# Kernel tuning notes

Measured on AMD Instinct MI355X. Metric: run time of the kernel, lower is better.

## Reference

```python
import jax, jax.numpy as jnp
import numpy as np

K = 20
HID = 64
NUM_CLASSES = 50
BIG = 1e10  # effectively-infinite distance for self-loop exclusion


def knn_idx(x, k):
    # x: [N, d] -> idx: [N, k] indices of k nearest neighbors in feature space (excluding self)
    sq = jnp.sum(x * x, axis=1)
    dist = sq[:, None] + sq[None, :] - 2.0 * (x @ x.T)  # [N, N]
    n = x.shape[0]
    dist = dist.at[jnp.arange(n), jnp.arange(n)].set(BIG)
    _, idx = jax.lax.top_k(-dist, k)
    return idx


def edge_conv(x, k, W, b):
    # DynamicEdgeConv: message = relu(Linear(cat[x_i, x_j - x_i])), aggr = max over k neighbors
    idx = knn_idx(x, k)                      # [N, k]
    xj = x[idx]                              # [N, k, d] neighbor gather
    xi = jnp.broadcast_to(x[:, None, :], xj.shape)
    feat = jnp.concatenate([xi, xj - xi], axis=-1)   # [N, k, 2d]
    h = jax.nn.relu(jnp.einsum('nkf,fo->nko', feat, W) + b)
    return jnp.max(h, axis=1)                # [N, out]


def setup_inputs() -> dict:
    key = jax.random.key(0)
    ks = jax.random.split(key, 16)
    def lin(kw, fan_in, fan_out):
        s = 1.0 / np.sqrt(fan_in)
        return jax.random.uniform(kw, (fan_in, fan_out), jnp.float32, -s, s)
    inp = {
        'x':  jax.random.normal(ks[0], (8192, 3), jnp.float32),
        'W1': lin(ks[1], 2 * 3, HID),      'b1': jnp.zeros((HID,), jnp.float32),
        'W2': lin(ks[2], 2 * HID, HID),    'b2': jnp.zeros((HID,), jnp.float32),
        'W3': lin(ks[3], 2 * HID, HID),    'b3': jnp.zeros((HID,), jnp.float32),
        'Wl': lin(ks[4], 3 * HID, 1024),   'bl': jnp.zeros((1024,), jnp.float32),
        'Wm1': lin(ks[5], 1024, 256),      'bm1': jnp.zeros((256,), jnp.float32),
        'Wm2': lin(ks[6], 256, 128),       'bm2': jnp.zeros((128,), jnp.float32),
        'Wo': lin(ks[7], 128, NUM_CLASSES),'bo': jnp.zeros((NUM_CLASSES,), jnp.float32),
    }
    return inp


def reference(x, W1, b1, W2, b2, W3, b3, Wl, bl, Wm1, bm1, Wm2, bm2, Wo, bo):
    x1 = edge_conv(x, K, W1, b1)     # [N, 64], kNN on raw 3-D points
    x2 = edge_conv(x1, K, W2, b2)    # [N, 64], kNN recomputed in feature space
    x3 = edge_conv(x2, K, W3, b3)    # [N, 64]
    h = jnp.concatenate([x1, x2, x3], axis=1)            # [N, 192]
    h = jax.nn.relu(h @ Wl + bl)                         # lin1: MLP([192, 1024])
    h = jax.nn.relu(h @ Wm1 + bm1)                       # MLP([1024, 256]) (dropout: eval mode)
    h = jax.nn.relu(h @ Wm2 + bm2)                       # MLP([256, 128])
    out = h @ Wo + bo                                    # final Linear
    return jax.nn.log_softmax(out, axis=-1)
```

## Files before the change

### kernel.cpp

```cpp
#include <hip/hip_runtime.h>
#include <math.h>

#define NPTS 8192
#define KNN 20
#define NLISTS 32
#define JSPLIT 8

#define OFF_SQ   0
#define OFF_IDX  8192
#define OFF_A    172032
#define OFF_B    696320
#define OFF_CAT  1220608
#define OFF_H1   2793472
#define OFF_H2   11182080
#define OFF_H3   13279232
#define OFF_PART OFF_H1
#define OFF_PACK (OFF_H1 + 5242880)
#define PACK_ELEMS 262144
#define OFF_WT   OFF_A

typedef __attribute__((ext_vector_type(8))) short bf16x8;
typedef __attribute__((ext_vector_type(16))) float f32x16;

__device__ inline unsigned umed3(unsigned a, unsigned b, unsigned c) {
    unsigned d;
    asm("v_med3_u32 %0, %1, %2, %3" : "=v"(d) : "v"(a), "v"(b), "v"(c));
    return d;
}

__device__ inline unsigned short f2bf(float f) {
    unsigned u = __float_as_uint(f);
    u += 0x7FFFu + ((u >> 16) & 1u);
    return (unsigned short)(u >> 16);
}

template<int D>
__global__ __launch_bounds__(256)
void sqnorm_kernel(const float* __restrict__ X, int stride, float* __restrict__ sq) {
    int n = blockIdx.x * blockDim.x + threadIdx.x;
    if (n < NPTS) {
        float s = 0.f;
        #pragma unroll
        for (int f = 0; f < D; ++f) {
            float v = X[(size_t)n * stride + f];
            s = fmaf(v, v, s);
        }
        sq[n] = s;
    }
}

template<int D, int KP>
__global__ __launch_bounds__(256)
void prepack_kernel(const float* __restrict__ X, int stride,
                    unsigned short* __restrict__ Xhi, unsigned short* __restrict__ Xlo,
                    unsigned short* __restrict__ Yhi, unsigned short* __restrict__ Ylo) {
    int t2 = blockIdx.x * 256 + threadIdx.x;
    int t = t2 * 2;
    int n = t >> (KP == 64 ? 6 : 4);
    int k = t & (KP - 1);
    float xv[2];
    xv[0] = (k     < D) ? X[(size_t)n * stride + k]     : 0.f;
    xv[1] = (k + 1 < D) ? X[(size_t)n * stride + k + 1] : 0.f;
    ushort2 hx, lx, hy, ly;
    unsigned short* hxp = (unsigned short*)&hx;
    unsigned short* lxp = (unsigned short*)&lx;
    unsigned short* hyp = (unsigned short*)&hy;
    unsigned short* lyp = (unsigned short*)&ly;
    #pragma unroll
    for (int e = 0; e < 2; ++e) {
        float x = xv[e];
        unsigned short hi = f2bf(x);
        float hif = __uint_as_float((unsigned)hi << 16);
        unsigned short lo = f2bf(x - hif);
        float y = -2.f * x;
        unsigned short yhi = f2bf(y);
        float yhif = __uint_as_float((unsigned)yhi << 16);
        unsigned short ylo = f2bf(y - yhif);
        hxp[e] = hi; lxp[e] = lo; hyp[e] = yhi; lyp[e] = ylo;
    }
    *(ushort2*)&Xhi[t] = hx;
    *(ushort2*)&Xlo[t] = lx;
    *(ushort2*)&Yhi[t] = hy;
    *(ushort2*)&Ylo[t] = ly;
}

template<int K, int NBITS>
__global__ __launch_bounds__(256)
void prepack_w(const float* __restrict__ W,
               unsigned short* __restrict__ Thi, unsigned short* __restrict__ Tlo) {
    const int N = 1 << NBITS;
    int t = blockIdx.x * 256 + threadIdx.x;
    int k = t >> NBITS, n = t & (N - 1);
    float x = W[t];
    unsigned short hi = f2bf(x);
    float hif = __uint_as_float((unsigned)hi << 16);
    unsigned short lo = f2bf(x - hif);
    Thi[(size_t)n * K + k] = hi;
    Tlo[(size_t)n * K + k] = lo;
}

template<int KP>
__global__ __launch_bounds__(256, 4)
void knnA_mfma(const unsigned short* __restrict__ Yhi, const unsigned short* __restrict__ Ylo,
               const unsigned short* __restrict__ Xhi, const unsigned short* __restrict__ Xlo,
               const float* __restrict__ sq, unsigned int* __restrict__ part) {
    constexpr int NS = KP / 16;
    constexpr int NT = NPTS / JSPLIT / 4 / 32;
    const int wave = threadIdx.x >> 6, lane = threadIdx.x & 63;
    const int col = lane & 31;
    const int h   = lane >> 5;
    const int i0  = blockIdx.x * 32;
    const int bi  = i0 + col;
    const int jbase = blockIdx.y * (NPTS / JSPLIT) + wave * (NPTS / JSPLIT / 4);

    bf16x8 bhi[NS], blo[NS];
    #pragma unroll
    for (int s = 0; s < NS; ++s) {
        bhi[s] = *(const bf16x8*)&Xhi[(size_t)bi * KP + s * 16 + h * 8];
        blo[s] = *(const bf16x8*)&Xlo[(size_t)bi * KP + s * 16 + h * 8];
    }
    const float sqi = sq[bi];

    unsigned top[KNN];
    #pragma unroll
    for (int k = 0; k < KNN; ++k) top[k] = 0xFFFFFFFFu;

    for (int jt = 0; jt < NT; ++jt) {
        const int j0 = jbase + jt * 32;
        const int aj = j0 + col;
        f32x16 C;
        #pragma unroll
        for (int r = 0; r < 16; ++r) C[r] = 0.f;
        #pragma unroll
        for (int s = 0; s < NS; ++s) {
            bf16x8 ahi = *(const bf16x8*)&Yhi[(size_t)aj * KP + s * 16 + h * 8];
            bf16x8 alo = *(const bf16x8*)&Ylo[(size_t)aj * KP + s * 16 + h * 8];
            C = __builtin_amdgcn_mfma_f32_32x32x16_bf16(ahi, bhi[s], C, 0, 0, 0);
            C = __builtin_amdgcn_mfma_f32_32x32x16_bf16(ahi, blo[s], C, 0, 0, 0);
            C = __builtin_amdgcn_mfma_f32_32x32x16_bf16(alo, bhi[s], C, 0, 0, 0);
        }
        #pragma unroll
        for (int q = 0; q < 4; ++q) {
            const int jq = j0 + h * 4 + q * 8;
            const float4 s4 = *(const float4*)&sq[jq];
            float bb[4] = {sqi + s4.x, sqi + s4.y, sqi + s4.z, sqi + s4.w};
            #pragma unroll
            for (int t = 0; t < 4; ++t) {
                const int r = q * 4 + t;
                const int j = jq + t;
                float d = bb[t] + C[r];
                unsigned db = __float_as_uint(d);
                unsigned ord = db ^ ((unsigned)((int)db >> 31) | 0x80000000u);
                unsigned key = (ord & 0xFFFFE000u) | (unsigned)j;
                if (j == bi) key = 0xFFFFFFFFu;
                #pragma unroll
                for (int p = KNN - 1; p >= 1; --p)
                    top[p] = umed3(key, top[p - 1], top[p]);
                top[0] = min(top[0], key);
            }
        }
    }

    {
        bool done = false;
        #pragma unroll
        for (int k = 0; k < KNN; ++k) {
            unsigned c = __shfl_xor(top[k], 32);
            if (!done) done = __all(c >= top[KNN - 1]);
            if (!done) {
                #pragma unroll
                for (int p = KNN - 1; p >= 1; --p)
                    top[p] = umed3(c, top[p - 1], top[p]);
                top[0] = min(top[0], c);
            }
        }
    }

    if (h == 0) {
        unsigned* o = part + ((size_t)bi * NLISTS + blockIdx.y * 4 + wave) * KNN;
        #pragma unroll
        for (int k = 0; k < KNN; ++k) o[k] = top[k];
    }
}

__global__ __launch_bounds__(256)
void knnB_kernel(const unsigned int* __restrict__ part, int* __restrict__ idx_out) {
    const int wave = threadIdx.x >> 6, lane = threadIdx.x & 63;
    const int half = lane >> 5;
    const int l = lane & 31;
    const int row = (blockIdx.x * 4 + wave) * 2 + half;

    unsigned top[KNN];
    const unsigned* p = part + ((size_t)row * NLISTS + l) * KNN;
    #pragma unroll
    for (int k = 0; k < KNN; k += 4) {
        uint4 v = *(const uint4*)(p + k);
        top[k] = v.x; top[k + 1] = v.y; top[k + 2] = v.z; top[k + 3] = v.w;
    }

    #pragma unroll
    for (int mi = 0; mi < 5; ++mi) {
        const int m = 1 << mi;
        bool done = false;
        #pragma unroll
        for (int k = 0; k < KNN; ++k) {
            unsigned c = __shfl_xor(top[k], m);
            if (!done) done = __all(c >= top[KNN - 1]);
            if (!done) {
                #pragma unroll
                for (int q = KNN - 1; q >= 1; --q)
                    top[q] = umed3(c, top[q - 1], top[q]);
                top[0] = min(top[0], c);
            }
        }
    }

    if (l == 0) {
        #pragma unroll
        for (int k = 0; k < KNN; ++k)
            idx_out[(size_t)row * KNN + k] = (int)(top[k] & 0x1FFFu);
    }
}

template<int D>
__global__ __launch_bounds__(256)
void featAB_kernel(const float* __restrict__ X, int stride, const float* __restrict__ W,
                   float* __restrict__ A, float* __restrict__ B) {
    const int wave = threadIdx.x >> 6, lane = threadIdx.x & 63;
    const int n = blockIdx.x * 4 + wave;
    float a = 0.f, b = 0.f;
    const float* xp = X + (size_t)n * stride;
    #pragma unroll
    for (int f = 0; f < D; ++f) {
        float xf = xp[f];
        a = fmaf(xf, W[(size_t)f * 64 + lane], a);
        b = fmaf(xf, W[(size_t)(D + f) * 64 + lane], b);
    }
    A[(size_t)n * 64 + lane] = a;
    B[(size_t)n * 64 + lane] = b;
}

__global__ __launch_bounds__(256)
void edge_agg_kernel(const float* __restrict__ A, const float* __restrict__ B,
                     const int* __restrict__ idx, const float* __restrict__ bias,
                     float* __restrict__ out, int ostride) {
    const int wave = threadIdx.x >> 6, lane = threadIdx.x & 63;
    const int n = blockIdx.x * 4 + wave;
    const float base = A[(size_t)n * 64 + lane] - B[(size_t)n * 64 + lane] + bias[lane];
    float m = -INFINITY;
    #pragma unroll 4
    for (int k = 0; k < KNN; ++k) {
        int j = idx[(size_t)n * KNN + k];
        m = fmaxf(m, base + B[(size_t)j * 64 + lane]);
    }
    out[(size_t)n * ostride + lane] = fmaxf(m, 0.f);
}

template<int K, int N, int CTW>
__global__ __launch_bounds__(256, 3)
void gemm_mfma_relu(const float* __restrict__ A,
                    const unsigned short* __restrict__ Whi, const unsigned short* __restrict__ Wlo,
                    const float* __restrict__ bias, float* __restrict__ C) {
    const int wave = threadIdx.x >> 6, lane = threadIdx.x & 63;
    const int col = lane & 31, h = lane >> 5;
    const int r0 = blockIdx.x * 32;
    const int nb = blockIdx.y * (CTW * 128) + wave * (CTW * 32);
    const float* arow = A + (size_t)(r0 + col) * K + h * 8;

    f32x16 acc[CTW];
    #pragma unroll
    for (int c = 0; c < CTW; ++c)
        #pragma unroll
        for (int r = 0; r < 16; ++r) acc[c][r] = 0.f;

    #pragma unroll 4
    for (int s = 0; s < K / 16; ++s) {
        float4 f0 = *(const float4*)(arow + s * 16);
        float4 f1 = *(const float4*)(arow + s * 16 + 4);
        bf16x8 ahi, alo;
        {
            float xv[8] = {f0.x, f0.y, f0.z, f0.w, f1.x, f1.y, f1.z, f1.w};
            #pragma unroll
            for (int e = 0; e < 8; ++e) {
                unsigned u = __float_as_uint(xv[e]);
                ahi[e] = (short)(u >> 16);
                float d = xv[e] - __uint_as_float(u & 0xFFFF0000u);
                alo[e] = (short)(__float_as_uint(d) >> 16);
            }
        }
        #pragma unroll
        for (int c = 0; c < CTW; ++c) {
            const size_t wb = (size_t)(nb + c * 32 + col) * K + s * 16 + h * 8;
            bf16x8 bhi = *(const bf16x8*)&Whi[wb];
            bf16x8 blo = *(const bf16x8*)&Wlo[wb];
            acc[c] = __builtin_amdgcn_mfma_f32_32x32x16_bf16(ahi, bhi, acc[c], 0, 0, 0);
            acc[c] = __builtin_amdgcn_mfma_f32_32x32x16_bf16(alo, bhi, acc[c], 0, 0, 0);
            acc[c] = __builtin_amdgcn_mfma_f32_32x32x16_bf16(ahi, blo, acc[c], 0, 0, 0);
        }
    }

    #pragma unroll
    for (int c = 0; c < CTW; ++c) {
        const int n = nb + c * 32 + col;
        const float b = bias[n];
        #pragma unroll
        for (int q = 0; q < 4; ++q)
            #pragma unroll
            for (int t = 0; t < 4; ++t) {
                const int rl = 4 * h + 8 * q + t;
                C[(size_t)(r0 + rl) * N + n] = fmaxf(acc[c][q * 4 + t] + b, 0.f);
            }
    }
}

__global__ __launch_bounds__(256)
void final_kernel(const float* __restrict__ H, const float* __restrict__ Wo,
                  const float* __restrict__ bo, float* __restrict__ out) {
    const int wave = threadIdx.x >> 6, lane = threadIdx.x & 63;
    const int n = blockIdx.x * 4 + wave;
    float v = -INFINITY;
    if (lane < 50) {
        float a = bo[lane];
        const float* h = H + (size_t)n * 128;
        #pragma unroll 4
        for (int f = 0; f < 128; ++f) a = fmaf(h[f], Wo[f * 50 + lane], a);
        v = a;
    }
    float mx = v;
    #pragma unroll
    for (int off = 32; off; off >>= 1) mx = fmaxf(mx, __shfl_xor(mx, off));
    float e = (lane < 50) ? expf(v - mx) : 0.f;
    float s = e;
    #pragma unroll
    for (int off = 32; off; off >>= 1) s += __shfl_xor(s, off);
    if (lane < 50) out[(size_t)n * 50 + lane] = v - mx - logf(s);
}

extern "C" void kernel_launch(void* const* d_in, const int* in_sizes, int n_in,
                              void* d_out, int out_size, void* d_ws, size_t ws_size,
                              hipStream_t stream) {
    const float* x   = (const float*)d_in[0];
    const float* W1  = (const float*)d_in[1];
    const float* b1  = (const float*)d_in[2];
    const float* W2  = (const float*)d_in[3];
    const float* b2  = (const float*)d_in[4];
    const float* W3  = (const float*)d_in[5];
    const float* b3  = (const float*)d_in[6];
    const float* Wl  = (const float*)d_in[7];
    const float* bl  = (const float*)d_in[8];
    const float* Wm1 = (const float*)d_in[9];
    const float* bm1 = (const float*)d_in[10];
    const float* Wm2 = (const float*)d_in[11];
    const float* bm2 = (const float*)d_in[12];
    const float* Wo  = (const float*)d_in[13];
    const float* bo  = (const float*)d_in[14];

    float* ws   = (float*)d_ws;
    float* sq   = ws + OFF_SQ;
    int*   idx  = (int*)(ws + OFF_IDX);
    float* Abuf = ws + OFF_A;
    float* Bbuf = ws + OFF_B;
    float* cat  = ws + OFF_CAT;
    float* h1   = ws + OFF_H1;
    unsigned int* part = (unsigned int*)(ws + OFF_PART);
    unsigned short* Phi = (unsigned short*)(ws + OFF_PACK);
    unsigned short* Plo = (unsigned short*)(ws + OFF_PACK + PACK_ELEMS);
    unsigned short* Qhi = (unsigned short*)(ws + OFF_PACK + 2 * PACK_ELEMS);
    unsigned short* Qlo = (unsigned short*)(ws + OFF_PACK + 3 * PACK_ELEMS);
    float* h2   = ws + OFF_H2;
    float* h3   = ws + OFF_H3;
    unsigned short* WlT_hi  = (unsigned short*)(ws + OFF_WT);
    unsigned short* WlT_lo  = (unsigned short*)(ws + OFF_WT + 98304);
    unsigned short* Wm1T_hi = (unsigned short*)(ws + OFF_WT + 196608);
    unsigned short* Wm1T_lo = (unsigned short*)(ws + OFF_WT + 327680);
    unsigned short* Wm2T_hi = (unsigned short*)(ws + OFF_WT + 458752);
    unsigned short* Wm2T_lo = (unsigned short*)(ws + OFF_WT + 475136);
    float* out  = (float*)d_out;

    dim3 b256(256);
    dim3 gknn(256, JSPLIT);

    sqnorm_kernel<3><<<32, b256, 0, stream>>>(x, 3, sq);
    prepack_kernel<3, 16><<<256, b256, 0, stream>>>(x, 3, Phi, Plo, Qhi, Qlo);
    knnA_mfma<16><<<gknn, b256, 0, stream>>>(Qhi, Qlo, Phi, Plo, sq, part);
    knnB_kernel<<<1024, b256, 0, stream>>>(part, idx);
    featAB_kernel<3><<<2048, b256, 0, stream>>>(x, 3, W1, Abuf, Bbuf);
    edge_agg_kernel<<<2048, b256, 0, stream>>>(Abuf, Bbuf, idx, b1, cat + 0, 192);

    sqnorm_kernel<64><<<32, b256, 0, stream>>>(cat + 0, 192, sq);
    prepack_kernel<64, 64><<<1024, b256, 0, stream>>>(cat + 0, 192, Phi, Plo, Qhi, Qlo);
    knnA_mfma<64><<<gknn, b256, 0, stream>>>(Qhi, Qlo, Phi, Plo, sq, part);
    knnB_kernel<<<1024, b256, 0, stream>>>(part, idx);
    featAB_kernel<64><<<2048, b256, 0, stream>>>(cat + 0, 192, W2, Abuf, Bbuf);
    edge_agg_kernel<<<2048, b256, 0, stream>>>(Abuf, Bbuf, idx, b2, cat + 64, 192);

    sqnorm_kernel<64><<<32, b256, 0, stream>>>(cat + 64, 192, sq);
    prepack_kernel<64, 64><<<1024, b256, 0, stream>>>(cat + 64, 192, Phi, Plo, Qhi, Qlo);
    knnA_mfma<64><<<gknn, b256, 0, stream>>>(Qhi, Qlo, Phi, Plo, sq, part);
    knnB_kernel<<<1024, b256, 0, stream>>>(part, idx);
    featAB_kernel<64><<<2048, b256, 0, stream>>>(cat + 64, 192, W3, Abuf, Bbuf);
    edge_agg_kernel<<<2048, b256, 0, stream>>>(Abuf, Bbuf, idx, b3, cat + 128, 192);

    prepack_w<192, 10><<<768, b256, 0, stream>>>(Wl, WlT_hi, WlT_lo);
    prepack_w<1024, 8><<<1024, b256, 0, stream>>>(Wm1, Wm1T_hi, Wm1T_lo);
    prepack_w<256, 7><<<128, b256, 0, stream>>>(Wm2, Wm2T_hi, Wm2T_lo);

    dim3 g1(256, 4);
    gemm_mfma_relu<192, 1024, 2><<<g1, b256, 0, stream>>>(cat, WlT_hi, WlT_lo, bl, h1);
    dim3 g2(256, 1);
    gemm_mfma_relu<1024, 256, 2><<<g2, b256, 0, stream>>>(h1, Wm1T_hi, Wm1T_lo, bm1, h2);
    dim3 g3(256, 1);
    gemm_mfma_relu<256, 128, 1><<<g3, b256, 0, stream>>>(h2, Wm2T_hi, Wm2T_lo, bm2, h3);
    final_kernel<<<2048, b256, 0, stream>>>(h3, Wo, bo, out);
}
```

Measured before the change: 539.4 us.

## Fuse kNN prepack into edge aggregation and restructure kNN wave tiling

Edge aggregation for layers 1 and 2 now also computes the squared norms and the bf16 hi/lo split operands for the next kNN, replacing the separate sqnorm and prepack launches. The kNN kernel gives each wave its own 32 query rows over a 256-point j block shared by the block's waves, changing reuse of the neighbor tiles. It also initialises the MFMA accumulator with the norm sums and clamps distances at zero so the raw float bits serve as the sort key. This saves launches and an extra pass over features, at the cost of more work in the edge kernel and different cache behaviour in kNN.

```diff
diff --git a/kernel.cpp b/kernel.cpp
--- a/kernel.cpp
+++ b/kernel.cpp
@@ -4,7 +4,6 @@
 #define NPTS 8192
 #define KNN 20
 #define NLISTS 32
-#define JSPLIT 8
 
 #define OFF_SQ   0
 #define OFF_IDX  8192
@@ -105,13 +104,12 @@
                const unsigned short* __restrict__ Xhi, const unsigned short* __restrict__ Xlo,
                const float* __restrict__ sq, unsigned int* __restrict__ part) {
     constexpr int NS = KP / 16;
-    constexpr int NT = NPTS / JSPLIT / 4 / 32;
+    constexpr int NT = 8;
     const int wave = threadIdx.x >> 6, lane = threadIdx.x & 63;
     const int col = lane & 31;
     const int h   = lane >> 5;
-    const int i0  = blockIdx.x * 32;
-    const int bi  = i0 + col;
-    const int jbase = blockIdx.y * (NPTS / JSPLIT) + wave * (NPTS / JSPLIT / 4);
+    const int bi  = (blockIdx.x * 4 + wave) * 32 + col;
+    const int jbase = blockIdx.y * 256;
 
     bf16x8 bhi[NS], blo[NS];
     #pragma unroll
@@ -130,7 +128,13 @@
         const int aj = j0 + col;
         f32x16 C;
         #pragma unroll
-        for (int r = 0; r < 16; ++r) C[r] = 0.f;
+        for (int q = 0; q < 4; ++q) {
+            const float4 s4 = *(const float4*)&sq[j0 + h * 4 + q * 8];
+            C[q * 4 + 0] = sqi + s4.x;
+            C[q * 4 + 1] = sqi + s4.y;
+            C[q * 4 + 2] = sqi + s4.z;
+            C[q * 4 + 3] = sqi + s4.w;
+        }
         #pragma unroll
         for (int s = 0; s < NS; ++s) {
             bf16x8 ahi = *(const bf16x8*)&Yhi[(size_t)aj * KP + s * 16 + h * 8];
@@ -142,16 +146,11 @@
         #pragma unroll
         for (int q = 0; q < 4; ++q) {
             const int jq = j0 + h * 4 + q * 8;
-            const float4 s4 = *(const float4*)&sq[jq];
-            float bb[4] = {sqi + s4.x, sqi + s4.y, sqi + s4.z, sqi + s4.w};
             #pragma unroll
             for (int t = 0; t < 4; ++t) {
-                const int r = q * 4 + t;
                 const int j = jq + t;
-                float d = bb[t] + C[r];
-                unsigned db = __float_as_uint(d);
-                unsigned ord = db ^ ((unsigned)((int)db >> 31) | 0x80000000u);
-                unsigned key = (ord & 0xFFFFE000u) | (unsigned)j;
+                float d = fmaxf(C[q * 4 + t], 0.f);
+                unsigned key = (__float_as_uint(d) & 0xFFFFE000u) | (unsigned)j;
                 if (j == bi) key = 0xFFFFFFFFu;
                 #pragma unroll
                 for (int p = KNN - 1; p >= 1; --p)
@@ -177,7 +176,7 @@
     }
 
     if (h == 0) {
-        unsigned* o = part + ((size_t)bi * NLISTS + blockIdx.y * 4 + wave) * KNN;
+        unsigned* o = part + ((size_t)bi * NLISTS + blockIdx.y) * KNN;
         #pragma unroll
         for (int k = 0; k < KNN; ++k) o[k] = top[k];
     }
@@ -238,6 +237,43 @@
     }
     A[(size_t)n * 64 + lane] = a;
     B[(size_t)n * 64 + lane] = b;
+}
+
+__global__ __launch_bounds__(256)
+void edge_fuse_kernel(const float* __restrict__ A, const float* __restrict__ B,
+                      const int* __restrict__ idx, const float* __restrict__ bias,
+                      float* __restrict__ out, int ostride,
+                      float* __restrict__ sqo,
+                      unsigned short* __restrict__ Xhi, unsigned short* __restrict__ Xlo,
+                      unsigned short* __restrict__ Yhi, unsigned short* __restrict__ Ylo) {
+    const int wave = threadIdx.x >> 6, lane = threadIdx.x & 63;
+    const int n = blockIdx.x * 4 + wave;
+    const float base = A[(size_t)n * 64 + lane] - B[(size_t)n * 64 + lane] + bias[lane];
+    float m = -INFINITY;
+    #pragma unroll 4
+    for (int k = 0; k < KNN; ++k) {
+        int j = idx[(size_t)n * KNN + k];
+        m = fmaxf(m, base + B[(size_t)j * 64 + lane]);
+    }
+    m = fmaxf(m, 0.f);
+    out[(size_t)n * ostride + lane] = m;
+
+    float s = m * m;
+    #pragma unroll
+    for (int off = 32; off; off >>= 1) s += __shfl_xor(s, off);
+    if (lane == 0) sqo[n] = s;
+
+    unsigned short hi = f2bf(m);
+    float hif = __uint_as_float((unsigned)hi << 16);
+    unsigned short lo = f2bf(m - hif);
+    float y = -2.f * m;
+    unsigned short yhi = f2bf(y);
+    float yhif = __uint_as_float((unsigned)yhi << 16);
+    unsigned short ylo = f2bf(y - yhif);
+    Xhi[(size_t)n * 64 + lane] = hi;
+    Xlo[(size_t)n * 64 + lane] = lo;
+    Yhi[(size_t)n * 64 + lane] = yhi;
+    Ylo[(size_t)n * 64 + lane] = ylo;
 }
 
 __global__ __launch_bounds__(256)
@@ -378,24 +414,22 @@
     float* out  = (float*)d_out;
 
     dim3 b256(256);
-    dim3 gknn(256, JSPLIT);
+    dim3 gknn(64, 32);
 
     sqnorm_kernel<3><<<32, b256, 0, stream>>>(x, 3, sq);
     prepack_kernel<3, 16><<<256, b256, 0, stream>>>(x, 3, Phi, Plo, Qhi, Qlo);
     knnA_mfma<16><<<gknn, b256, 0, stream>>>(Qhi, Qlo, Phi, Plo, sq, part);
     knnB_kernel<<<1024, b256, 0, stream>>>(part, idx);
     featAB_kernel<3><<<2048, b256, 0, stream>>>(x, 3, W1, Abuf, Bbuf);
-    edge_agg_kernel<<<2048, b256, 0, stream>>>(Abuf, Bbuf, idx, b1, cat + 0, 192);
-
-    sqnorm_kernel<64><<<32, b256, 0, stream>>>(cat + 0, 192, sq);
-    prepack_kernel<64, 64><<<1024, b256, 0, stream>>>(cat + 0, 192, Phi, Plo, Qhi, Qlo);
+    edge_fuse_kernel<<<2048, b256, 0, stream>>>(Abuf, Bbuf, idx, b1, cat + 0, 192,
+                                                sq, Phi, Plo, Qhi, Qlo);
+
     knnA_mfma<64><<<gknn, b256, 0, stream>>>(Qhi, Qlo, Phi, Plo, sq, part);
     knnB_kernel<<<1024, b256, 0, stream>>>(part, idx);
     featAB_kernel<64><<<2048, b256, 0, stream>>>(cat + 0, 192, W2, Abuf, Bbuf);
-    edge_agg_kernel<<<2048, b256, 0, stream>>>(Abuf, Bbuf, idx, b2, cat + 64, 192);
-
-    sqnorm_kernel<64><<<32, b256, 0, stream>>>(cat + 64, 192, sq);
-    prepack_kernel<64, 64><<<1024, b256, 0, stream>>>(cat + 64, 192, Phi, Plo, Qhi, Qlo);
+    edge_fuse_kernel<<<2048, b256, 0, stream>>>(Abuf, Bbuf, idx, b2, cat + 64, 192,
+                                                sq, Phi, Plo, Qhi, Qlo);
+
     knnA_mfma<64><<<gknn, b256, 0, stream>>>(Qhi, Qlo, Phi, Plo, sq, part);
     knnB_kernel<<<1024, b256, 0, stream>>>(part, idx);
     featAB_kernel<64><<<2048, b256, 0, stream>>>(cat + 64, 192, W3, Abuf, Bbuf);
```

Measured after the change: 523.0 us. 1.03x faster.
